# Performance work log

Hardware: AMD Instinct MI355X
Metric: run time of the kernel (lower is better)

Reference implementation:

```python
import jax, jax.numpy as jnp
import numpy as np

D_MODEL = 1024
STATE = 64
HEADS = 8
EXPAND = 2
INNER = EXPAND * D_MODEL          # 2048
HEAD_DIM = INNER // HEADS         # 256
PROJ_OUT = 2 * INNER + 2 * STATE + HEADS  # z, x, B, C, dt
BATCH, SEQ = 2, 1024
EPS = 1e-5


def setup_inputs() -> dict:
    key = jax.random.key(0)
    ks = jax.random.split(key, 6)
    g = lambda k, shape, sc: jax.random.normal(k, shape, jnp.float32) * sc
    return {
        "input_tensor": jax.random.normal(ks[0], (BATCH, SEQ, D_MODEL), jnp.float32),
        "ln_gamma": jnp.ones((D_MODEL,), jnp.float32),
        "ln_beta": jnp.zeros((D_MODEL,), jnp.float32),
        "W_in": g(ks[1], (D_MODEL, PROJ_OUT), 0.02),
        "b_in": jnp.zeros((PROJ_OUT,), jnp.float32),
        "A_log": jnp.log(jnp.arange(1, HEADS + 1, dtype=jnp.float32)),
        "D_skip": jnp.ones((HEADS,), jnp.float32),
        "dt_bias": g(ks[2], (HEADS,), 0.1),
        "W_out": g(ks[3], (INNER, D_MODEL), 0.02),
        "b_out": jnp.zeros((D_MODEL,), jnp.float32),
    }


def _layer_norm(x, gamma, beta):
    mu = jnp.mean(x, axis=-1, keepdims=True)
    xc = x - mu
    var = jnp.mean(xc * xc, axis=-1, keepdims=True)
    return xc * jax.lax.rsqrt(var + EPS) * gamma + beta


def _mamba2(u, W_in, b_in, A_log, D_skip, dt_bias, W_out, b_out):
    B, L, _ = u.shape
    zxbcdt = u @ W_in + b_in                                    # [B,L,PROJ_OUT]
    z = zxbcdt[..., :INNER]                                     # gate [B,L,INNER]
    xs = zxbcdt[..., INNER:2 * INNER].reshape(B, L, HEADS, HEAD_DIM)
    Bm = zxbcdt[..., 2 * INNER:2 * INNER + STATE]               # [B,L,N]
    Cm = zxbcdt[..., 2 * INNER + STATE:2 * INNER + 2 * STATE]   # [B,L,N]
    dt = jax.nn.softplus(zxbcdt[..., 2 * INNER + 2 * STATE:] + dt_bias)  # [B,L,H]

    A = -jnp.exp(A_log)                                         # [H], negative
    decay = jnp.exp(dt * A)                                     # [B,L,H]
    dtx = dt[..., None] * xs                                    # [B,L,H,P]

    # selective scan over time; state h: [B,H,P,N]
    def step(h, inp):
        dec_t, dtx_t, B_t, C_t = inp                            # [B,H],[B,H,P],[B,N],[B,N]
        h = dec_t[:, :, None, None] * h + dtx_t[..., None] * B_t[:, None, None, :]
        y = jnp.einsum('bhpn,bn->bhp', h, C_t)
        return h, y

    h0 = jnp.zeros((B, HEADS, HEAD_DIM, STATE), u.dtype)
    scan_in = (
        jnp.moveaxis(decay, 1, 0),   # [L,B,H]
        jnp.moveaxis(dtx, 1, 0),     # [L,B,H,P]
        jnp.moveaxis(Bm, 1, 0),      # [L,B,N]
        jnp.moveaxis(Cm, 1, 0),      # [L,B,N]
    )
    _, ys = jax.lax.scan(step, h0, scan_in)                     # [L,B,H,P]
    y = jnp.moveaxis(ys, 0, 1)                                  # [B,L,H,P]
    y = y + D_skip[None, None, :, None] * xs                    # skip connection
    y = y.reshape(B, L, INNER) * jax.nn.silu(z)                 # gated
    return y @ W_out + b_out


def reference(input_tensor, ln_gamma, ln_beta, W_in, b_in, A_log, D_skip, dt_bias, W_out, b_out):
    normed = _layer_norm(input_tensor, ln_gamma, ln_beta)
    out = _mamba2(normed, W_in, b_in, A_log, D_skip, dt_bias, W_out, b_out)
    return input_tensor + out
```

## Files before the change

### kernel.cpp

```cpp
#include <hip/hip_runtime.h>
#include <math.h>

#define D_MODEL 1024
#define STATE 64
#define HEADS 8
#define INNER 2048
#define HEAD_DIM 256
#define PROJ_OUT 4232
#define DT_OFF  4224
#define NPAD 4352
#define BATCH 2
#define SEQ 1024
#define NROWS (BATCH*SEQ)
#define EPS 1e-5f
#define BH (BATCH * HEADS)
#define LQ 32
#define NCH (SEQ / LQ)

typedef short s16x8 __attribute__((ext_vector_type(8)));
typedef float f32x4 __attribute__((ext_vector_type(4)));

#define LDS_AS(p) ((__attribute__((address_space(3))) void*)(p))
#define GLB_AS(p) ((const __attribute__((address_space(1))) void*)(p))

__device__ inline unsigned short f2bf(float f) {
    unsigned int u = __float_as_uint(f);
    unsigned int r = (u + 0x7fffu + ((u >> 16) & 1u)) >> 16;
    return (unsigned short)r;
}
__device__ inline float bf2f(unsigned short s) {
    return __uint_as_float(((unsigned int)s) << 16);
}
__device__ inline f32x4 mfma16(s16x8 a, s16x8 b, f32x4 c) {
    return __builtin_amdgcn_mfma_f32_16x16x32_bf16(a, b, c, 0, 0, 0);
}

__global__ __launch_bounds__(256) void prep_kernel(
    const float* __restrict__ x, const float* __restrict__ gamma,
    const float* __restrict__ beta,
    const float* __restrict__ W_in, const float* __restrict__ W_out,
    unsigned short* __restrict__ normed, unsigned short* __restrict__ WT,
    unsigned short* __restrict__ WoT)
{
    constexpr int T1 = (NPAD / 32) * (D_MODEL / 32);
    constexpr int T2 = (D_MODEL / 32) * (INNER / 32);
    __shared__ float tile[32][33];
    __shared__ float ls[4], lq[4];
    const int bid = blockIdx.x;
    const int tid = threadIdx.x;

    if (bid < T1 + T2) {
        const float* in;
        unsigned short* out;
        int R, C, bx, by;
        if (bid < T1) {
            in = W_in; out = WT; R = D_MODEL; C = PROJ_OUT;
            bx = bid % (NPAD / 32); by = bid / (NPAD / 32);
        } else {
            int t = bid - T1;
            in = W_out; out = WoT; R = INNER; C = D_MODEL;
            bx = t % (D_MODEL / 32); by = t / (D_MODEL / 32);
        }
        int c0 = bx * 32, r0 = by * 32;
        int tx = tid & 31, ty = tid >> 5;
        #pragma unroll
        for (int i = 0; i < 4; ++i) {
            int r = ty + i * 8;
            int gc = c0 + tx;
            tile[r][tx] = (gc < C) ? in[(size_t)(r0 + r) * C + gc] : 0.f;
        }
        __syncthreads();
        #pragma unroll
        for (int i = 0; i < 4; ++i) {
            int oc = ty + i * 8;
            out[(size_t)(c0 + oc) * R + r0 + tx] = f2bf(tile[tx][oc]);
        }
    } else {
        int t = bid - T1 - T2;
        int wave = tid >> 6, lane = tid & 63;
        #pragma unroll
        for (int rr = 0; rr < 2; ++rr) {
            int row = t * 2 + rr;
            const float4* xr = (const float4*)(x + (size_t)row * D_MODEL);
            float4 v = xr[tid];
            float s  = v.x + v.y + v.z + v.w;
            float sq = v.x*v.x + v.y*v.y + v.z*v.z + v.w*v.w;
            #pragma unroll
            for (int off = 32; off > 0; off >>= 1) {
                s  += __shfl_down(s,  off, 64);
                sq += __shfl_down(sq, off, 64);
            }
            if (lane == 0) { ls[wave] = s; lq[wave] = sq; }
            __syncthreads();
            s  = ls[0] + ls[1] + ls[2] + ls[3];
            sq = lq[0] + lq[1] + lq[2] + lq[3];
            float mu  = s * (1.f / D_MODEL);
            float var = sq * (1.f / D_MODEL) - mu * mu;
            float rs  = rsqrtf(var + EPS);
            float4 g  = ((const float4*)gamma)[tid];
            float4 bb = ((const float4*)beta)[tid];
            ushort4 o;
            o.x = f2bf((v.x - mu) * rs * g.x + bb.x);
            o.y = f2bf((v.y - mu) * rs * g.y + bb.y);
            o.z = f2bf((v.z - mu) * rs * g.z + bb.z);
            o.w = f2bf((v.w - mu) * rs * g.w + bb.w);
            ((ushort4*)(normed + (size_t)row * D_MODEL))[tid] = o;
            __syncthreads();
        }
    }
}

template<int BM, int BN, int RECT_N, int RECT_M, int CHX,
         bool HAS_ADD, bool GUARD_N, bool OUT_BF16>
__global__ __launch_bounds__(256) void gemm_bf16(
    const unsigned short* __restrict__ A, const unsigned short* __restrict__ BT,
    const float* __restrict__ bias, const float* __restrict__ add,
    float* __restrict__ C, unsigned short* __restrict__ Cb,
    float* __restrict__ dtb, int Nreal, int Nstride, int K)
{
    constexpr int FM = BM / 32;
    constexpr int FN = BN / 32;
    constexpr int NL = BM / 64 + BN / 64;
    __shared__ unsigned short Asm[3][BM * 32];
    __shared__ unsigned short Bsm[3][BN * 32];
    const int tid = threadIdx.x;
    const int l = tid & 63, w = tid >> 6;
    const int lr = l & 15, lk = l >> 4;

    const int bid = blockIdx.x;
    const int c  = bid & 7;
    const int e  = bid >> 3;
    const int cx = c % CHX, cy = c / CHX;
    const int nt = cx * RECT_N + e % RECT_N;
    const int mt = cy * RECT_M + e / RECT_N;
    const int m0 = mt * BM, n0 = nt * BN;
    const int wm = w >> 1, wn = w & 1;

    f32x4 acc[FM][FN] = {};

    const unsigned short* Abase = A  + (size_t)(m0 + lr) * K + lk * 8;
    const unsigned short* Bbase = BT + (size_t)(n0 + lr) * K + lk * 8;

    auto stage = [&](int buf, int k0) {
        #pragma unroll
        for (int i = 0; i < BM / 64; ++i) {
            int mb = w + 4 * i;
            __builtin_amdgcn_global_load_lds(
                GLB_AS(Abase + (size_t)mb * 16 * K + k0),
                LDS_AS(&Asm[buf][mb * 512]), 16, 0, 0);
        }
        #pragma unroll
        for (int i = 0; i < BN / 64; ++i) {
            int nb = w + 4 * i;
            __builtin_amdgcn_global_load_lds(
                GLB_AS(Bbase + (size_t)nb * 16 * K + k0),
                LDS_AS(&Bsm[buf][nb * 512]), 16, 0, 0);
        }
    };

    stage(0, 0);
    stage(1, 32);
    stage(2, 64);
    int cur = 0;
    for (int k0 = 0; k0 < K; k0 += 32) {
        if (k0 + 96 <= K) {
            if constexpr (NL == 4)
                asm volatile("s_waitcnt vmcnt(8)" ::: "memory");
            else
                asm volatile("s_waitcnt vmcnt(4)" ::: "memory");
        } else if (k0 + 64 <= K) {
            if constexpr (NL == 4)
                asm volatile("s_waitcnt vmcnt(4)" ::: "memory");
            else
                asm volatile("s_waitcnt vmcnt(2)" ::: "memory");
        } else {
            asm volatile("s_waitcnt vmcnt(0)" ::: "memory");
        }
        __builtin_amdgcn_s_barrier();
        __builtin_amdgcn_sched_barrier(0);
        s16x8 af[FM], bfv[FN];
        #pragma unroll
        for (int i = 0; i < FM; ++i)
            af[i] = *(const s16x8*)&Asm[cur][((wm * FM + i) * 64 + l) * 8];
        #pragma unroll
        for (int j = 0; j < FN; ++j)
            bfv[j] = *(const s16x8*)&Bsm[cur][((wn * FN + j) * 64 + l) * 8];
        #pragma unroll
        for (int i = 0; i < FM; ++i)
            #pragma unroll
            for (int j = 0; j < FN; ++j)
                acc[i][j] = mfma16(af[i], bfv[j], acc[i][j]);
        __builtin_amdgcn_s_barrier();
        if (k0 + 128 <= K) stage(cur, k0 + 96);
        cur = (cur == 2) ? 0 : cur + 1;
    }

    #pragma unroll
    for (int i = 0; i < FM; ++i) {
        int row = m0 + (wm * FM + i) * 16 + lk * 4;
        #pragma unroll
        for (int j = 0; j < FN; ++j) {
            int col = n0 + (wn * FN + j) * 16 + lr;
            if (GUARD_N && col >= Nreal) continue;
            float bv = bias[col];
            #pragma unroll
            for (int r = 0; r < 4; ++r) {
                float v = acc[i][j][r] + bv;
                if (HAS_ADD) v += add[(size_t)(row + r) * Nstride + col];
                if (OUT_BF16) {
                    Cb[(size_t)(row + r) * Nstride + col] = f2bf(v);
                    if (col >= DT_OFF)
                        dtb[(size_t)(row + r) * HEADS + (col - DT_OFF)] = v;
                } else {
                    C[(size_t)(row + r) * Nstride + col] = v;
                }
            }
        }
    }
}

__global__ __launch_bounds__(256) void ssd_pass1(
    const unsigned short* __restrict__ zx, const float* __restrict__ dtbuf,
    const float* __restrict__ A_log, const float* __restrict__ dt_bias,
    unsigned short* __restrict__ Sbuf, float* __restrict__ Dk)
{
    __shared__ float w1s[LQ];
    __shared__ unsigned short xT[HEAD_DIM * LQ];
    __shared__ unsigned short BpT[STATE * LQ];
    int blk = blockIdx.x;
    int bh = blk >> 5, ck = blk & (NCH - 1);
    int b = bh >> 3, h = bh & 7;
    int tid = threadIdx.x;
    int l = tid & 63, w = tid >> 6;
    int lr = l & 15, lk = l >> 4;
    float a = -expf(A_log[h]);
    int t0 = ck * LQ;
    const unsigned short* zrow = zx + (size_t)(b * SEQ + t0) * PROJ_OUT;

    if (w == 0) {
        int tl = l & 31;
        float dtr = dtbuf[(size_t)(b * SEQ + t0 + tl) * HEADS + h] + dt_bias[h];
        float dtv = (dtr > 20.f) ? dtr : log1pf(expf(dtr));
        float c = dtv;
        #pragma unroll
        for (int off = 1; off < 32; off <<= 1) {
            float v = __shfl_up(c, off, 64);
            if ((l & 31) >= off) c += v;
        }
        float c31 = __shfl(c, 31, 64);
        if (l < 32) {
            w1s[l] = dtv * expf(a * (c31 - c));
            if (l == 31) Dk[bh * NCH + ck] = expf(a * c31);
        }
    }
    {
        int p = tid;
        const unsigned short* xp = zrow + INNER + h * HEAD_DIM + p;
        int sw = (p & 3) << 3;
        #pragma unroll
        for (int tp = 0; tp < 16; ++tp) {
            unsigned int x0 = xp[(size_t)(2 * tp) * PROJ_OUT];
            unsigned int x1 = xp[(size_t)(2 * tp + 1) * PROJ_OUT];
            *(unsigned int*)&xT[p * LQ + ((2 * tp) ^ sw)] = x0 | (x1 << 16);
        }
    }
    __syncthreads();
    #pragma unroll
    for (int i = 0; i < 8; ++i) {
        int e = i * 256 + tid;
        int t = e >> 6, n = e & 63;
        float v = bf2f(zrow[(size_t)t * PROJ_OUT + 2 * INNER + n]) * w1s[t];
        BpT[n * LQ + (t ^ ((n & 3) << 3))] = f2bf(v);
    }
    __syncthreads();

    f32x4 acc[4][4] = {};
    {
        int krun = lk * 8;
        s16x8 bfr[4];
        #pragma unroll
        for (int j = 0; j < 4; ++j) {
            int n = j * 16 + lr;
            bfr[j] = *(const s16x8*)&BpT[n * LQ + (krun ^ ((n & 3) << 3))];
        }
        #pragma unroll
        for (int i = 0; i < 4; ++i) {
            int p = (w * 4 + i) * 16 + lr;
            s16x8 afr = *(const s16x8*)&xT[p * LQ + (krun ^ ((p & 3) << 3))];
            #pragma unroll
            for (int j = 0; j < 4; ++j)
                acc[i][j] = mfma16(afr, bfr[j], acc[i][j]);
        }
    }
    unsigned short* sp = Sbuf + ((size_t)bh * NCH + ck) * (STATE * HEAD_DIM);
    #pragma unroll
    for (int i = 0; i < 4; ++i) {
        int p = (w * 4 + i) * 16 + lk * 4;
        #pragma unroll
        for (int j = 0; j < 4; ++j) {
            int n = j * 16 + lr;
            #pragma unroll
            for (int r = 0; r < 4; ++r)
                sp[(size_t)(p + r) * STATE + n] = f2bf(acc[i][j][r]);
        }
    }
}

template<int NCHq>
__global__ __launch_bounds__(256) void scan_combine(
    unsigned short* __restrict__ Sbuf, const float* __restrict__ Dk)
{
    int bh = blockIdx.y;
    int e  = blockIdx.x * 256 + threadIdx.x;
    size_t base = (size_t)bh * NCHq * (STATE * HEAD_DIM) + e;
    float h = 0.f;
    #pragma unroll 8
    for (int k = 0; k < NCHq; ++k) {
        size_t idx = base + (size_t)k * (STATE * HEAD_DIM);
        float s = bf2f(Sbuf[idx]);
        Sbuf[idx] = f2bf(h);
        h = Dk[bh * NCHq + k] * h + s;
    }
}

__global__ __launch_bounds__(256) void ssd_pass2(
    const unsigned short* __restrict__ zx, const float* __restrict__ dtbuf,
    const float* __restrict__ A_log, const float* __restrict__ D_skip,
    const float* __restrict__ dt_bias,
    const unsigned short* __restrict__ Sbuf, unsigned short* __restrict__ yg)
{
    __shared__ float dts[LQ], cums[LQ];
    __shared__ unsigned short xT[HEAD_DIM * LQ];
    __shared__ unsigned short Cm[LQ * STATE];
    __shared__ unsigned short Cd[LQ * STATE];
    __shared__ unsigned short Bm[LQ * STATE];
    __shared__ unsigned short Pp[LQ * LQ];
    int blk = blockIdx.x;
    int bh = blk >> 5, ck = blk & (NCH - 1);
    int b = bh >> 3, h = bh & 7;
    int tid = threadIdx.x;
    int l = tid & 63, w = tid >> 6;
    int lr = l & 15, lk = l >> 4;
    float a = -expf(A_log[h]);
    float dsk = D_skip[h];
    int t0 = ck * LQ;
    const unsigned short* zrow = zx + (size_t)(b * SEQ + t0) * PROJ_OUT;

    if (w == 0) {
        int tl = l & 31;
        float dtr = dtbuf[(size_t)(b * SEQ + t0 + tl) * HEADS + h] + dt_bias[h];
        float dtv = (dtr > 20.f) ? dtr : log1pf(expf(dtr));
        float c = dtv;
        #pragma unroll
        for (int off = 1; off < 32; off <<= 1) {
            float v = __shfl_up(c, off, 64);
            if ((l & 31) >= off) c += v;
        }
        if (l < 32) { dts[l] = dtv; cums[l] = c; }
    }
    {
        int p = tid;
        const unsigned short* xp = zrow + INNER + h * HEAD_DIM + p;
        int sw = (p & 3) << 3;
        #pragma unroll
        for (int tp = 0; tp < 16; ++tp) {
            unsigned int x0 = xp[(size_t)(2 * tp) * PROJ_OUT];
            unsigned int x1 = xp[(size_t)(2 * tp + 1) * PROJ_OUT];
            *(unsigned int*)&xT[p * LQ + ((2 * tp) ^ sw)] = x0 | (x1 << 16);
        }
    }
    __syncthreads();
    #pragma unroll
    for (int i = 0; i < 8; ++i) {
        int e = i * 256 + tid;
        int t = e >> 6, n = e & 63;
        int sn = n ^ ((t & 7) << 3);
        unsigned short cv = zrow[(size_t)t * PROJ_OUT + 2 * INNER + STATE + n];
        Cm[t * STATE + sn] = cv;
        Cd[t * STATE + sn] = f2bf(bf2f(cv) * expf(a * cums[t]));
        Bm[t * STATE + sn] = zrow[(size_t)t * PROJ_OUT + 2 * INNER + n];
    }
    __syncthreads();

    const unsigned short* hbase = Sbuf + ((size_t)bh * NCH + ck) * (STATE * HEAD_DIM);
    s16x8 h0f[4][2];
    #pragma unroll
    for (int j = 0; j < 4; ++j) {
        int p = w * 64 + j * 16 + lr;
        #pragma unroll
        for (int kk = 0; kk < 2; ++kk)
            h0f[j][kk] = *(const s16x8*)&hbase[(size_t)p * STATE + kk * 32 + lk * 8];
    }

    f32x4 pa = {};
    #pragma unroll
    for (int kk = 0; kk < 2; ++kk) {
        int krun = kk * 32 + lk * 8;
        int tA = (w >> 1) * 16 + lr;
        int sB = (w & 1) * 16 + lr;
        s16x8 afr = *(const s16x8*)&Cm[tA * STATE + (krun ^ ((tA & 7) << 3))];
        s16x8 bfr = *(const s16x8*)&Bm[sB * STATE + (krun ^ ((sB & 7) << 3))];
        pa = mfma16(afr, bfr, pa);
    }
    #pragma unroll
    for (int r = 0; r < 4; ++r) {
        int t = (w >> 1) * 16 + lk * 4 + r;
        int s = (w & 1) * 16 + lr;
        float sc = (s <= t) ? dts[s] * expf(a * (cums[t] - cums[s])) : 0.f;
        Pp[t * LQ + (s ^ ((t & 3) << 3))] = f2bf(pa[r] * sc);
    }
    __syncthreads();

    f32x4 ya[2][4] = {};
    {
        int krun = lk * 8;
        s16x8 bfr[4];
        #pragma unroll
        for (int j = 0; j < 4; ++j) {
            int p = w * 64 + j * 16 + lr;
            bfr[j] = *(const s16x8*)&xT[p * LQ + (krun ^ ((p & 3) << 3))];
        }
        #pragma unroll
        for (int i = 0; i < 2; ++i) {
            int t = i * 16 + lr;
            s16x8 afr = *(const s16x8*)&Pp[t * LQ + (krun ^ ((t & 3) << 3))];
            #pragma unroll
            for (int j = 0; j < 4; ++j)
                ya[i][j] = mfma16(afr, bfr[j], ya[i][j]);
        }
    }
    #pragma unroll
    for (int kk = 0; kk < 2; ++kk) {
        int krun = kk * 32 + lk * 8;
        #pragma unroll
        for (int i = 0; i < 2; ++i) {
            int t = i * 16 + lr;
            s16x8 afr = *(const s16x8*)&Cd[t * STATE + (krun ^ ((t & 7) << 3))];
            #pragma unroll
            for (int j = 0; j < 4; ++j)
                ya[i][j] = mfma16(afr, h0f[j][kk], ya[i][j]);
        }
    }

    #pragma unroll
    for (int i = 0; i < 2; ++i) {
        #pragma unroll
        for (int r = 0; r < 4; ++r) {
            int t = i * 16 + lk * 4 + r;
            #pragma unroll
            for (int j = 0; j < 4; ++j) {
                int p = w * 64 + j * 16 + lr;
                float xv = bf2f(xT[p * LQ + (t ^ ((p & 3) << 3))]);
                float z  = bf2f(zrow[(size_t)t * PROJ_OUT + h * HEAD_DIM + p]);
                float y = ya[i][j][r] + dsk * xv;
                float gate = z / (1.f + expf(-z));
                yg[(size_t)(b * SEQ + t0 + t) * INNER + h * HEAD_DIM + p] = f2bf(y * gate);
            }
        }
    }
}

__global__ __launch_bounds__(256) void scan_serial(
    const unsigned short* __restrict__ zx, const float* __restrict__ dtbuf,
    const float* __restrict__ A_log, const float* __restrict__ D_skip,
    const float* __restrict__ dt_bias,
    unsigned short* __restrict__ yg)
{
    int bh = blockIdx.x;
    int b  = bh >> 3, h = bh & 7;
    int p  = threadIdx.x;
    float a   = -expf(A_log[h]);
    float dsk = D_skip[h];
    float dtb = dt_bias[h];

    float hs[STATE];
    #pragma unroll
    for (int n = 0; n < STATE; ++n) hs[n] = 0.f;

    for (int t = 0; t < SEQ; ++t) {
        const unsigned short* row = zx + (size_t)(b * SEQ + t) * PROJ_OUT;
        float dtr = dtbuf[(size_t)(b * SEQ + t) * HEADS + h] + dtb;
        float dt  = (dtr > 20.f) ? dtr : log1pf(expf(dtr));
        float dec = expf(dt * a);
        float x   = bf2f(row[INNER + h * HEAD_DIM + p]);
        float z   = bf2f(row[h * HEAD_DIM + p]);
        float dtx = dt * x;
        #pragma unroll
        for (int n = 0; n < STATE; ++n)
            hs[n] = dec * hs[n] + dtx * bf2f(row[2 * INNER + n]);
        float y0 = 0.f;
        #pragma unroll
        for (int n = 0; n < STATE; ++n)
            y0 += hs[n] * bf2f(row[2 * INNER + STATE + n]);
        float y = y0 + dsk * x;
        float gate = z / (1.f + expf(-z));
        yg[(size_t)(b * SEQ + t) * INNER + h * HEAD_DIM + p] = f2bf(y * gate);
    }
}

extern "C" void kernel_launch(void* const* d_in, const int* in_sizes, int n_in,
                              void* d_out, int out_size, void* d_ws, size_t ws_size,
                              hipStream_t stream) {
    const float* input  = (const float*)d_in[0];
    const float* gamma  = (const float*)d_in[1];
    const float* beta   = (const float*)d_in[2];
    const float* W_in   = (const float*)d_in[3];
    const float* b_in   = (const float*)d_in[4];
    const float* A_log  = (const float*)d_in[5];
    const float* D_skip = (const float*)d_in[6];
    const float* dt_b   = (const float*)d_in[7];
    const float* W_out  = (const float*)d_in[8];
    const float* b_out  = (const float*)d_in[9];
    float* out = (float*)d_out;

    char* ws = (char*)d_ws;
    size_t off = 0;
    unsigned short* normed_bf = (unsigned short*)(ws + off); off += (size_t)NROWS * D_MODEL * 2;
    unsigned short* zx        = (unsigned short*)(ws + off); off += (size_t)NROWS * PROJ_OUT * 2;
    float*          dtbuf     = (float*)(ws + off);          off += (size_t)NROWS * HEADS * 4;
    unsigned short* yg        = (unsigned short*)(ws + off); off += (size_t)NROWS * INNER * 2;
    unsigned short* WT        = (unsigned short*)(ws + off); off += (size_t)NPAD * D_MODEL * 2;
    unsigned short* WoT       = (unsigned short*)(ws + off); off += (size_t)D_MODEL * INNER * 2;
    unsigned short* Sbuf      = (unsigned short*)(ws + off); off += (size_t)BH * NCH * STATE * HEAD_DIM * 2;
    off = (off + 255) & ~(size_t)255;
    float*          Dk        = (float*)(ws + off);          off += (size_t)BH * NCH * 4;
    bool ssd = (off <= ws_size);

    constexpr int T1 = (NPAD / 32) * (D_MODEL / 32);
    constexpr int T2 = (D_MODEL / 32) * (INNER / 32);
    constexpr int T3 = NROWS / 2;
    prep_kernel<<<T1 + T2 + T3, 256, 0, stream>>>(
        input, gamma, beta, W_in, W_out, normed_bf, WT, WoT);

    gemm_bf16<128, 128, 17, 4, 2, false, true, true><<<544, 256, 0, stream>>>(
        normed_bf, WT, b_in, nullptr, nullptr, zx, dtbuf, PROJ_OUT, PROJ_OUT, D_MODEL);

    if (ssd) {
        ssd_pass1<<<BH * NCH, 256, 0, stream>>>(zx, dtbuf, A_log, dt_b, Sbuf, Dk);
        dim3 gc(STATE * HEAD_DIM / 256, BH);
        scan_combine<NCH><<<gc, 256, 0, stream>>>(Sbuf, Dk);
        ssd_pass2<<<BH * NCH, 256, 0, stream>>>(zx, dtbuf, A_log, D_skip, dt_b, Sbuf, yg);
    } else {
        scan_serial<<<BH, 256, 0, stream>>>(zx, dtbuf, A_log, D_skip, dt_b, yg);
    }

    gemm_bf16<64, 64, 16, 4, 1, true, false, false><<<512, 256, 0, stream>>>(
        yg, WoT, b_out, input, out, nullptr, nullptr, D_MODEL, D_MODEL, INNER);
}
```

Before: 131.1 us.

## Switch GEMM mainloop to K=64 steps with double buffering

```diff
diff --git a/kernel.cpp b/kernel.cpp
--- a/kernel.cpp
+++ b/kernel.cpp
@@ -120,9 +120,11 @@
 {
     constexpr int FM = BM / 32;
     constexpr int FN = BN / 32;
-    constexpr int NL = BM / 64 + BN / 64;
-    __shared__ unsigned short Asm[3][BM * 32];
-    __shared__ unsigned short Bsm[3][BN * 32];
+    constexpr int MFRAG = BM / 16;
+    constexpr int NFRAG = BN / 16;
+    constexpr int NL = (BM + BN) / 32;
+    __shared__ unsigned short Asm[2][BM * 64];
+    __shared__ unsigned short Bsm[2][BN * 64];
     const int tid = threadIdx.x;
     const int l = tid & 63, w = tid >> 6;
     const int lr = l & 15, lk = l >> 4;
@@ -138,61 +140,59 @@
 
     f32x4 acc[FM][FN] = {};
 
-    const unsigned short* Abase = A  + (size_t)(m0 + lr) * K + lk * 8;
-    const unsigned short* Bbase = BT + (size_t)(n0 + lr) * K + lk * 8;
-
     auto stage = [&](int buf, int k0) {
         #pragma unroll
-        for (int i = 0; i < BM / 64; ++i) {
-            int mb = w + 4 * i;
+        for (int i = 0; i < FM; ++i) {
+            int s = w * FM + i, k32 = s & 1, mf = s >> 1;
             __builtin_amdgcn_global_load_lds(
-                GLB_AS(Abase + (size_t)mb * 16 * K + k0),
-                LDS_AS(&Asm[buf][mb * 512]), 16, 0, 0);
-        }
-        #pragma unroll
-        for (int i = 0; i < BN / 64; ++i) {
-            int nb = w + 4 * i;
+                GLB_AS(A + (size_t)(m0 + mf * 16 + lr) * K + k0 + k32 * 32 + lk * 8),
+                LDS_AS(&Asm[buf][((k32 * MFRAG + mf) * 64 + l) * 8]), 16, 0, 0);
+        }
+        #pragma unroll
+        for (int i = 0; i < FN; ++i) {
+            int s = w * FN + i, k32 = s & 1, nf = s >> 1;
             __builtin_amdgcn_global_load_lds(
-                GLB_AS(Bbase + (size_t)nb * 16 * K + k0),
-                LDS_AS(&Bsm[buf][nb * 512]), 16, 0, 0);
+                GLB_AS(BT + (size_t)(n0 + nf * 16 + lr) * K + k0 + k32 * 32 + lk * 8),
+                LDS_AS(&Bsm[buf][((k32 * NFRAG + nf) * 64 + l) * 8]), 16, 0, 0);
         }
     };
 
     stage(0, 0);
-    stage(1, 32);
-    stage(2, 64);
+    if (K > 64) stage(1, 64);
     int cur = 0;
-    for (int k0 = 0; k0 < K; k0 += 32) {
-        if (k0 + 96 <= K) {
-            if constexpr (NL == 4)
+    for (int k0 = 0; k0 < K; k0 += 64) {
+        if (k0 + 64 < K) {
+            if constexpr (NL == 8)
                 asm volatile("s_waitcnt vmcnt(8)" ::: "memory");
             else
                 asm volatile("s_waitcnt vmcnt(4)" ::: "memory");
-        } else if (k0 + 64 <= K) {
-            if constexpr (NL == 4)
-                asm volatile("s_waitcnt vmcnt(4)" ::: "memory");
-            else
-                asm volatile("s_waitcnt vmcnt(2)" ::: "memory");
         } else {
             asm volatile("s_waitcnt vmcnt(0)" ::: "memory");
         }
         __builtin_amdgcn_s_barrier();
         __builtin_amdgcn_sched_barrier(0);
-        s16x8 af[FM], bfv[FN];
-        #pragma unroll
-        for (int i = 0; i < FM; ++i)
-            af[i] = *(const s16x8*)&Asm[cur][((wm * FM + i) * 64 + l) * 8];
-        #pragma unroll
-        for (int j = 0; j < FN; ++j)
-            bfv[j] = *(const s16x8*)&Bsm[cur][((wn * FN + j) * 64 + l) * 8];
-        #pragma unroll
-        for (int i = 0; i < FM; ++i)
+        s16x8 af[2][FM], bfv[2][FN];
+        #pragma unroll
+        for (int kk = 0; kk < 2; ++kk) {
+            #pragma unroll
+            for (int i = 0; i < FM; ++i)
+                af[kk][i] = *(const s16x8*)
+                    &Asm[cur][((kk * MFRAG + wm * FM + i) * 64 + l) * 8];
             #pragma unroll
             for (int j = 0; j < FN; ++j)
-                acc[i][j] = mfma16(af[i], bfv[j], acc[i][j]);
+                bfv[kk][j] = *(const s16x8*)
+                    &Bsm[cur][((kk * NFRAG + wn * FN + j) * 64 + l) * 8];
+        }
+        #pragma unroll
+        for (int kk = 0; kk < 2; ++kk)
+            #pragma unroll
+            for (int i = 0; i < FM; ++i)
+                #pragma unroll
+                for (int j = 0; j < FN; ++j)
+                    acc[i][j] = mfma16(af[kk][i], bfv[kk][j], acc[i][j]);
         __builtin_amdgcn_s_barrier();
-        if (k0 + 128 <= K) stage(cur, k0 + 96);
-        cur = (cur == 2) ? 0 : cur + 1;
+        if (k0 + 128 < K) stage(cur, k0 + 128);
+        cur ^= 1;
     }
 
     #pragma unroll
```

After: 137.6 us. +5.0%, slower.

## Split SSD chunk kernels across head-dim halves to double block count

Applied to the files above, without the earlier changes.

```diff
diff --git a/kernel.cpp b/kernel.cpp
--- a/kernel.cpp
+++ b/kernel.cpp
@@ -16,6 +16,7 @@
 #define BH (BATCH * HEADS)
 #define LQ 32
 #define NCH (SEQ / LQ)
+#define PHALF 128
 
 typedef short s16x8 __attribute__((ext_vector_type(8)));
 typedef float f32x4 __attribute__((ext_vector_type(4)));
@@ -225,10 +226,12 @@
     unsigned short* __restrict__ Sbuf, float* __restrict__ Dk)
 {
     __shared__ float w1s[LQ];
-    __shared__ unsigned short xT[HEAD_DIM * LQ];
+    __shared__ unsigned short xT[PHALF * LQ];
     __shared__ unsigned short BpT[STATE * LQ];
     int blk = blockIdx.x;
-    int bh = blk >> 5, ck = blk & (NCH - 1);
+    int ph = blk & 1;
+    int ck = (blk >> 1) & (NCH - 1);
+    int bh = blk >> 6;
     int b = bh >> 3, h = bh & 7;
     int tid = threadIdx.x;
     int l = tid & 63, w = tid >> 6;
@@ -250,15 +253,17 @@
         float c31 = __shfl(c, 31, 64);
         if (l < 32) {
             w1s[l] = dtv * expf(a * (c31 - c));
-            if (l == 31) Dk[bh * NCH + ck] = expf(a * c31);
+            if (l == 31 && ph == 0) Dk[bh * NCH + ck] = expf(a * c31);
         }
     }
     {
-        int p = tid;
-        const unsigned short* xp = zrow + INNER + h * HEAD_DIM + p;
+        int p = tid & (PHALF - 1);
+        int half = tid >> 7;
+        const unsigned short* xp = zrow + INNER + h * HEAD_DIM + ph * PHALF + p;
         int sw = (p & 3) << 3;
         #pragma unroll
-        for (int tp = 0; tp < 16; ++tp) {
+        for (int i = 0; i < 8; ++i) {
+            int tp = half * 8 + i;
             unsigned int x0 = xp[(size_t)(2 * tp) * PROJ_OUT];
             unsigned int x1 = xp[(size_t)(2 * tp + 1) * PROJ_OUT];
             *(unsigned int*)&xT[p * LQ + ((2 * tp) ^ sw)] = x0 | (x1 << 16);
@@ -274,7 +279,7 @@
     }
     __syncthreads();
 
-    f32x4 acc[4][4] = {};
+    f32x4 acc[2][4] = {};
     {
         int krun = lk * 8;
         s16x8 bfr[4];
@@ -284,8 +289,8 @@
             bfr[j] = *(const s16x8*)&BpT[n * LQ + (krun ^ ((n & 3) << 3))];
         }
         #pragma unroll
-        for (int i = 0; i < 4; ++i) {
-            int p = (w * 4 + i) * 16 + lr;
+        for (int i = 0; i < 2; ++i) {
+            int p = (w * 2 + i) * 16 + lr;
             s16x8 afr = *(const s16x8*)&xT[p * LQ + (krun ^ ((p & 3) << 3))];
             #pragma unroll
             for (int j = 0; j < 4; ++j)
@@ -294,8 +299,8 @@
     }
     unsigned short* sp = Sbuf + ((size_t)bh * NCH + ck) * (STATE * HEAD_DIM);
     #pragma unroll
-    for (int i = 0; i < 4; ++i) {
-        int p = (w * 4 + i) * 16 + lk * 4;
+    for (int i = 0; i < 2; ++i) {
+        int p = ph * PHALF + (w * 2 + i) * 16 + lk * 4;
         #pragma unroll
         for (int j = 0; j < 4; ++j) {
             int n = j * 16 + lr;
@@ -330,13 +335,15 @@
     const unsigned short* __restrict__ Sbuf, unsigned short* __restrict__ yg)
 {
     __shared__ float dts[LQ], cums[LQ];
-    __shared__ unsigned short xT[HEAD_DIM * LQ];
+    __shared__ unsigned short xT[PHALF * LQ];
     __shared__ unsigned short Cm[LQ * STATE];
     __shared__ unsigned short Cd[LQ * STATE];
     __shared__ unsigned short Bm[LQ * STATE];
     __shared__ unsigned short Pp[LQ * LQ];
     int blk = blockIdx.x;
-    int bh = blk >> 5, ck = blk & (NCH - 1);
+    int ph = blk & 1;
+    int ck = (blk >> 1) & (NCH - 1);
+    int bh = blk >> 6;
     int b = bh >> 3, h = bh & 7;
     int tid = threadIdx.x;
     int l = tid & 63, w = tid >> 6;
@@ -359,11 +366,13 @@
         if (l < 32) { dts[l] = dtv; cums[l] = c; }
     }
     {
-        int p = tid;
-        const unsigned short* xp = zrow + INNER + h * HEAD_DIM + p;
+        int p = tid & (PHALF - 1);
+        int half = tid >> 7;
+        const unsigned short* xp = zrow + INNER + h * HEAD_DIM + ph * PHALF + p;
         int sw = (p & 3) << 3;
         #pragma unroll
-        for (int tp = 0; tp < 16; ++tp) {
+        for (int i = 0; i < 8; ++i) {
+            int tp = half * 8 + i;
             unsigned int x0 = xp[(size_t)(2 * tp) * PROJ_OUT];
             unsigned int x1 = xp[(size_t)(2 * tp + 1) * PROJ_OUT];
             *(unsigned int*)&xT[p * LQ + ((2 * tp) ^ sw)] = x0 | (x1 << 16);
@@ -383,10 +392,10 @@
     __syncthreads();
 
     const unsigned short* hbase = Sbuf + ((size_t)bh * NCH + ck) * (STATE * HEAD_DIM);
-    s16x8 h0f[4][2];
-    #pragma unroll
-    for (int j = 0; j < 4; ++j) {
-        int p = w * 64 + j * 16 + lr;
+    s16x8 h0f[2][2];
+    #pragma unroll
+    for (int j = 0; j < 2; ++j) {
+        int p = ph * PHALF + w * 32 + j * 16 + lr;
         #pragma unroll
         for (int kk = 0; kk < 2; ++kk)
             h0f[j][kk] = *(const s16x8*)&hbase[(size_t)p * STATE + kk * 32 + lk * 8];
@@ -411,13 +420,13 @@
     }
     __syncthreads();
 
-    f32x4 ya[2][4] = {};
+    f32x4 ya[2][2] = {};
     {
         int krun = lk * 8;
-        s16x8 bfr[4];
-        #pragma unroll
-        for (int j = 0; j < 4; ++j) {
-            int p = w * 64 + j * 16 + lr;
+        s16x8 bfr[2];
+        #pragma unroll
+        for (int j = 0; j < 2; ++j) {
+            int p = w * 32 + j * 16 + lr;
             bfr[j] = *(const s16x8*)&xT[p * LQ + (krun ^ ((p & 3) << 3))];
         }
         #pragma unroll
@@ -425,7 +434,7 @@
             int t = i * 16 + lr;
             s16x8 afr = *(const s16x8*)&Pp[t * LQ + (krun ^ ((t & 3) << 3))];
             #pragma unroll
-            for (int j = 0; j < 4; ++j)
+            for (int j = 0; j < 2; ++j)
                 ya[i][j] = mfma16(afr, bfr[j], ya[i][j]);
         }
     }
@@ -437,7 +446,7 @@
             int t = i * 16 + lr;
             s16x8 afr = *(const s16x8*)&Cd[t * STATE + (krun ^ ((t & 7) << 3))];
             #pragma unroll
-            for (int j = 0; j < 4; ++j)
+            for (int j = 0; j < 2; ++j)
                 ya[i][j] = mfma16(afr, h0f[j][kk], ya[i][j]);
         }
     }
@@ -448,9 +457,10 @@
         for (int r = 0; r < 4; ++r) {
             int t = i * 16 + lk * 4 + r;
             #pragma unroll
-            for (int j = 0; j < 4; ++j) {
-                int p = w * 64 + j * 16 + lr;
-                float xv = bf2f(xT[p * LQ + (t ^ ((p & 3) << 3))]);
+            for (int j = 0; j < 2; ++j) {
+                int p_loc = w * 32 + j * 16 + lr;
+                int p = ph * PHALF + p_loc;
+                float xv = bf2f(xT[p_loc * LQ + (t ^ ((p_loc & 3) << 3))]);
                 float z  = bf2f(zrow[(size_t)t * PROJ_OUT + h * HEAD_DIM + p]);
                 float y = ya[i][j][r] + dsk * xv;
                 float gate = z / (1.f + expf(-z));
@@ -536,10 +546,10 @@
         normed_bf, WT, b_in, nullptr, nullptr, zx, dtbuf, PROJ_OUT, PROJ_OUT, D_MODEL);
 
     if (ssd) {
-        ssd_pass1<<<BH * NCH, 256, 0, stream>>>(zx, dtbuf, A_log, dt_b, Sbuf, Dk);
+        ssd_pass1<<<BH * NCH * 2, 256, 0, stream>>>(zx, dtbuf, A_log, dt_b, Sbuf, Dk);
         dim3 gc(STATE * HEAD_DIM / 256, BH);
         scan_combine<NCH><<<gc, 256, 0, stream>>>(Sbuf, Dk);
-        ssd_pass2<<<BH * NCH, 256, 0, stream>>>(zx, dtbuf, A_log, D_skip, dt_b, Sbuf, yg);
+        ssd_pass2<<<BH * NCH * 2, 256, 0, stream>>>(zx, dtbuf, A_log, D_skip, dt_b, Sbuf, yg);
     } else {
         scan_serial<<<BH, 256, 0, stream>>>(zx, dtbuf, A_log, D_skip, dt_b, yg);
     }
```

Result: no change. 131.6 us (+0.4%).
